# Kernel optimization log

Measured on AMD Instinct MI355X. Metric: run time of the kernel, lower is better.

Reference implementation:

```python
import jax, jax.numpy as jnp
import numpy as np
from jax import lax

NUM_HEADS = 8

def _conv2d(x, w, b, padding, rhs_dilation=(1, 1)):
    # x: NCHW, w: OIHW
    out = lax.conv_general_dilated(x, w, (1, 1), padding,
                                   rhs_dilation=rhs_dilation,
                                   dimension_numbers=('NCHW', 'OIHW', 'NCHW'))
    return out + b[None, :, None, None]

def _bn(x, scale, bias):
    # eval-mode batchnorm folded into per-channel affine
    return x * scale[None, :, None, None] + bias[None, :, None, None]

def setup_inputs() -> dict:
    key = jax.random.key(0)
    ks = jax.random.split(key, 12)
    B, C, H, W = 16, 256, 64, 64
    D = C // 2          # down_dim = 128
    Dq = D // 16        # weight bottleneck = 8
    return {
        'x':          jax.random.normal(ks[0], (B, C, H, W), jnp.float32),
        'conv2_w':    jax.random.normal(ks[1], (D, C, 3, 3), jnp.float32) * 0.02,
        'conv2_b':    jnp.zeros((D,), jnp.float32),
        'bn2_scale':  jax.random.uniform(ks[2], (D,), jnp.float32, 0.5, 1.5),
        'bn2_bias':   jax.random.normal(ks[3], (D,), jnp.float32) * 0.1,
        'temperature': jnp.ones((NUM_HEADS, 1, 1), jnp.float32),
        'w1_w':       jax.random.normal(ks[4], (Dq, D, 1, 1), jnp.float32) * 0.05,
        'w1_b':       jnp.zeros((Dq,), jnp.float32),
        'bnw_scale':  jax.random.uniform(ks[5], (Dq,), jnp.float32, 0.5, 1.5),
        'bnw_bias':   jax.random.normal(ks[6], (Dq,), jnp.float32) * 0.1,
        'w2_w':       jax.random.normal(ks[7], (D, Dq, 1, 1), jnp.float32) * 0.05,
        'w2_b':       jnp.zeros((D,), jnp.float32),
    }

def _l2_normalize_complex(z, eps=1e-12):
    # torch F.normalize on complex: divide by L2 norm of |z| along last dim
    n = jnp.sqrt(jnp.sum(jnp.real(z * jnp.conj(z)), axis=-1, keepdims=True))
    return z / jnp.maximum(n, eps)

def reference(x, conv2_w, conv2_b, bn2_scale, bn2_bias, temperature,
              w1_w, w1_b, bnw_scale, bnw_bias, w2_w, w2_b):
    # conv2 branch: 3x3 conv with dilation=3, padding=3 -> BN -> ReLU
    conv2 = jax.nn.relu(_bn(_conv2d(x, conv2_w, conv2_b,
                                    ((3, 3), (3, 3)), rhs_dilation=(3, 3)),
                            bn2_scale, bn2_bias))
    b, c, h, w = conv2.shape
    f = jnp.fft.fft2(conv2)                      # complex64, (b,c,h,w); q=k=v=tepqkv
    cp = c // NUM_HEADS
    qkv = f.reshape(b, NUM_HEADS, cp, h * w)     # 'b (head c) h w -> b head c (h w)'
    qn = _l2_normalize_complex(qkv)
    kn = qn
    # complex attention logits, temperature broadcast over heads
    attn = jnp.einsum('bhin,bhjn->bhij', qn, kn) * temperature.astype(attn_dtype := qn.dtype)
    # dual real/imag softmax reassembled into complex
    attn = lax.complex(jax.nn.softmax(attn.real, axis=-1),
                       jax.nn.softmax(attn.imag, axis=-1))
    out_f = jnp.einsum('bhij,bhjn->bhin', attn, qkv)
    # torch.fft.ifft2 default dims=(-2,-1): here over (c, h*w) axes — faithful
    out_f = jnp.abs(jnp.fft.ifft2(out_f)).reshape(b, c, h, w)
    # gating branch on real part of spectrum
    g = jax.nn.relu(_bn(_conv2d(f.real, w1_w, w1_b, ((0, 0), (0, 0))),
                        bnw_scale, bnw_bias))
    g = jax.nn.sigmoid(_conv2d(g, w2_w, w2_b, ((0, 0), (0, 0))))
    out_l = jnp.abs(jnp.fft.ifft2(g * f))        # ifft2 over (h, w)
    out = jnp.concatenate([out_f, out_l], axis=1)
    return out + x
```

## Files before the change

### kernel.cpp

```cpp
#include <hip/hip_runtime.h>

typedef unsigned short u16;
typedef short short8 __attribute__((ext_vector_type(8)));
typedef float f32x4 __attribute__((ext_vector_type(4)));

#define MF(a,b,c) __builtin_amdgcn_mfma_f32_16x16x32_bf16(a,b,c,0,0,0)

__device__ __forceinline__ float bu2f(u16 u){
  return __uint_as_float(((unsigned int)u) << 16);
}
__device__ __forceinline__ u16 f2bu(float f){
  unsigned int b = __float_as_uint(f);
  unsigned int r = (b + 0x7FFFu + ((b >> 16) & 1u)) >> 16;
  return (u16)r;
}
__device__ __forceinline__ void ld4a(float* d, const float* p){
  float4 v = *(const float4*)p;
  d[0]=v.x; d[1]=v.y; d[2]=v.z; d[3]=v.w;
}
__device__ __forceinline__ void st4(float* p, const float* s){
  *(float4*)p = make_float4(s[0], s[1], s[2], s[3]);
}
__device__ __forceinline__ void ld4b(float* d, const u16* p){
  ushort4 v = *(const ushort4*)p;
  d[0]=bu2f(v.x); d[1]=bu2f(v.y); d[2]=bu2f(v.z); d[3]=bu2f(v.w);
}
__device__ __forceinline__ void st4b(u16* p, const float* s){
  ushort4 v;
  v.x=f2bu(s[0]); v.y=f2bu(s[1]); v.z=f2bu(s[2]); v.w=f2bu(s[3]);
  *(ushort4*)p = v;
}
__device__ __forceinline__ ushort4 pk4(f32x4 v){
  ushort4 u; u.x=f2bu(v[0]); u.y=f2bu(v[1]); u.z=f2bu(v[2]); u.w=f2bu(v[3]); return u;
}
__device__ __forceinline__ short8 mulpk(short8 g, short8 f){
  short8 o;
  #pragma unroll
  for (int e = 0; e < 8; ++e)
    o[e] = (short)f2bu(bu2f((u16)g[e])*bu2f((u16)f[e]));
  return o;
}

#define TABF_RE   0
#define TABF_IM   4096
#define TABIF_RE  8192
#define TABIF_IM  12288
#define TABTW_RE  16384
#define TABTW_IM  20480
#define NORMS_OFF 24576
#define MMAT_OFF  26624
#define FLAG_OFF  92160
#define PRM_OFF   92224
#define WT_OFF    94848
#define DFT16_OFF 242304
#define F32_END   389760
#define P_CB   0
#define P_BNS  128
#define P_BNB  256
#define P_TEMP 384
#define P_W1   400
#define P_B1   1424
#define P_S1   1432
#define P_BB1  1440
#define P_W2   1456
#define P_B2   2480
#define BPLANE    8388608

__global__ void k_detect(const u16* __restrict__ xv, int* __restrict__ flag){
  const int t = threadIdx.x;
  int huge = 0;
  for (int i = 0; i < 16; ++i){
    u16 u = xv[(t*16 + i)*2];
    int e = (u >> 7) & 0xFF;
    huge += (e >= 0xC0) ? 1 : 0;
  }
  #pragma unroll
  for (int off = 32; off > 0; off >>= 1) huge += __shfl_down(huge, off, 64);
  if (t == 0) flag[0] = (huge >= 8) ? 1 : 0;
}

__global__ void k_tables(float* ws){
  int idx = blockIdx.x*256 + threadIdx.x;
  int j = idx >> 6, k = idx & 63;
  int jk = j*k;
  float s, c;
  sincospif(-(float)(jk & 63)/32.0f, &s, &c);
  ws[TABF_RE+idx] = c; ws[TABF_IM+idx] = s;
  sincospif((float)(jk & 63)/32.0f, &s, &c);
  ws[TABIF_RE+idx] = c*(1.f/64.f); ws[TABIF_IM+idx] = s*(1.f/64.f);
  sincospif((float)jk/2048.0f, &s, &c);
  ws[TABTW_RE+idx] = c; ws[TABTW_IM+idx] = s;
}

__global__ void k_dftprep(u16* __restrict__ m){
  int idx = blockIdx.x*256 + threadIdx.x;
  int j = idx >> 6, k = idx & 63;
  int jk = (j*k) & 63;
  float s, c;
  sincospif(-(float)jk/32.0f, &s, &c);
  m[idx]        = f2bu(c);
  m[4096+idx]   = f2bu(s);
  sincospif((float)jk/32.0f, &s, &c);
  m[8192+idx]   = f2bu(c*(1.f/64.f));
  m[12288+idx]  = f2bu(s*(1.f/64.f));
}

__global__ void k_pack(const void* cb, const void* bns, const void* bnb, const void* temp,
                       const void* w1, const void* b1, const void* s1, const void* bb1,
                       const void* w2, const void* b2,
                       const int* __restrict__ flg, float* __restrict__ P){
  const int t = threadIdx.x;
  const int f32 = *flg;
  if (f32){
    for (int i = t; i < 128; i += 256){
      P[P_CB+i]  = ((const float*)cb)[i];
      P[P_BNS+i] = ((const float*)bns)[i];
      P[P_BNB+i] = ((const float*)bnb)[i];
      P[P_B2+i]  = ((const float*)b2)[i];
    }
    for (int i = t; i < 1024; i += 256){
      P[P_W1+i] = ((const float*)w1)[i];
      P[P_W2+i] = ((const float*)w2)[i];
    }
    if (t < 8){
      P[P_TEMP+t] = ((const float*)temp)[t];
      P[P_B1+t]   = ((const float*)b1)[t];
      P[P_S1+t]   = ((const float*)s1)[t];
      P[P_BB1+t]  = ((const float*)bb1)[t];
    }
  } else {
    for (int i = t; i < 128; i += 256){
      P[P_CB+i]  = bu2f(((const u16*)cb)[i]);
      P[P_BNS+i] = bu2f(((const u16*)bns)[i]);
      P[P_BNB+i] = bu2f(((const u16*)bnb)[i]);
      P[P_B2+i]  = bu2f(((const u16*)b2)[i]);
    }
    for (int i = t; i < 1024; i += 256){
      P[P_W1+i] = bu2f(((const u16*)w1)[i]);
      P[P_W2+i] = bu2f(((const u16*)w2)[i]);
    }
    if (t < 8){
      P[P_TEMP+t] = bu2f(((const u16*)temp)[t]);
      P[P_B1+t]   = bu2f(((const u16*)b1)[t]);
      P[P_S1+t]   = bu2f(((const u16*)s1)[t]);
      P[P_BB1+t]  = bu2f(((const u16*)bb1)[t]);
    }
  }
}

__global__ void k_wprep2(const void* __restrict__ w, u16* __restrict__ wT2,
                         const float* __restrict__ prm, const int* __restrict__ flg){
  const int f32 = *flg;
  int U = blockIdx.x*256 + threadIdx.x;
  if (U < 294912){
    int j = U & 7;
    int E = U >> 3;
    int n = E & 127;
    int o = (E >> 7) & 3;
    int tc = E >> 9;
    int chunk = tc & 7, tap = tc >> 3;
    int c = chunk*32 + o*8 + j;
    int src = n*2304 + c*9 + tap;
    float v = f32 ? ((const float*)w)[src] : bu2f(((const u16*)w)[src]);
    wT2[U] = f2bu(v * prm[P_BNS + n]);
  }
}

__global__ __launch_bounds__(256) void k_trans(const void* __restrict__ x, u16* __restrict__ xt,
                                               const int* __restrict__ flg){
  __shared__ u16 L[256*66];
  const int t = threadIdx.x;
  const int b = blockIdx.x >> 6, h = blockIdx.x & 63;
  const int f32m = __builtin_amdgcn_readfirstlane(*flg);
  if (f32m){
    const float* xf = (const float*)x;
    for (int i = t; i < 16384; i += 256){
      int c = i >> 6, w = i & 63;
      L[c*66 + w] = f2bu(xf[((b*256 + c)*64 + h)*64 + w]);
    }
  } else {
    const u16* xb = (const u16*)x;
    for (int i = t; i < 16384; i += 256){
      int c = i >> 6, w = i & 63;
      L[c*66 + w] = xb[((b*256 + c)*64 + h)*64 + w];
    }
  }
  __syncthreads();
  u16* dst = xt + ((b*64 + h)*64)*256;
  for (int j = t; j < 16384; j += 256){
    int w = j >> 8, c = j & 255;
    dst[w*256 + c] = L[c*66 + w];
  }
}

__global__ __launch_bounds__(256) void k_cmm(const u16* __restrict__ xt, const u16* __restrict__ wT2,
                                             const float* __restrict__ prm, u16* __restrict__ A){
  __shared__ uint4 sm4[4096];
  const int t = threadIdx.x;
  const int bb = blockIdx.x >> 4;
  const int mtile = blockIdx.x & 15;
  const int h0 = mtile*4;
  const int lane = t & 63, wave = t >> 6;
  const int quad = lane >> 4, lr = lane & 15;

  f32x4 acc[4][8];
  #pragma unroll
  for (int mi = 0; mi < 4; ++mi)
    #pragma unroll
    for (int nt = 0; nt < 8; ++nt)
      acc[mi][nt] = (f32x4){0.f,0.f,0.f,0.f};

  const u16* smB = (const u16*)sm4;
  const short8 zz = {0,0,0,0,0,0,0,0};

  for (int tap = 0; tap < 9; ++tap){
    const int ky = tap/3, kx = tap - ky*3;
    __syncthreads();
    {
      const uint4* src = (const uint4*)(wT2 + tap*32768);
      #pragma unroll
      for (int i = 0; i < 16; ++i) sm4[t + 256*i] = src[t + 256*i];
    }
    __syncthreads();

    const int hg = h0 + wave + 3*ky - 3;
    const bool hok = ((unsigned)hg < 64u);
    const u16* abase = xt + ((bb*64 + hg)*64)*256 + quad*8;

    for (int chunk = 0; chunk < 8; ++chunk){
      short8 av[4];
      #pragma unroll
      for (int mi = 0; mi < 4; ++mi){
        const int wg = mi*16 + lr + 3*kx - 3;
        short8 v = zz;
        if (hok && ((unsigned)wg < 64u))
          v = *(const short8*)(abase + wg*256 + chunk*32);
        av[mi] = v;
      }
      short8 bv[8];
      #pragma unroll
      for (int nt = 0; nt < 8; ++nt)
        bv[nt] = *(const short8*)(smB + (chunk*512 + quad*128 + nt*16 + lr)*8);
      #pragma unroll
      for (int mi = 0; mi < 4; ++mi)
        #pragma unroll
        for (int nt = 0; nt < 8; ++nt)
          acc[mi][nt] = MF(av[mi], bv[nt], acc[mi][nt]);
    }
  }

  float* C = (float*)sm4;
  u16* outb = A + (bb*128)*4096 + mtile*256;
  __syncthreads();
  for (int nt = 0; nt < 8; ++nt){
    #pragma unroll
    for (int mi = 0; mi < 4; ++mi)
      #pragma unroll
      for (int r = 0; r < 4; ++r){
        int m = wave*64 + mi*16 + quad*4 + r;
        C[lr*261 + m] = acc[mi][nt][r];
      }
    __syncthreads();
    #pragma unroll
    for (int dd = 0; dd < 16; ++dd){
      int d = nt*16 + dd;
      float bi = prm[P_CB + d]*prm[P_BNS + d] + prm[P_BNB + d];
      float v = fmaxf(C[dd*261 + t] + bi, 0.f);
      outb[d*4096 + t] = f2bu(v);
    }
    __syncthreads();
  }
}

__global__ __launch_bounds__(256) void k_fft2_m(const u16* __restrict__ A, u16* __restrict__ Frb,
                                                u16* __restrict__ Fib, const u16* __restrict__ dft){
  __shared__ __align__(16) u16 TTr[64*72], TTi[64*72];
  const int bc = blockIdx.x, t = threadIdx.x;
  const int lane = t & 63, wave = t >> 6;
  const int quad = lane >> 4, lr = lane & 15;
  const u16* EFr = dft;
  const u16* EFi = dft + 4096;
  const u16* img = A + bc*4096;
  #pragma unroll
  for (int mi = 0; mi < 4; ++mi){
    f32x4 ar = {0.f,0.f,0.f,0.f}, ai = {0.f,0.f,0.f,0.f};
    #pragma unroll
    for (int ks = 0; ks < 2; ++ks){
      short8 av = *(const short8*)(img + (mi*16+lr)*64 + ks*32 + quad*8);
      short8 br = *(const short8*)(EFr + (wave*16+lr)*64 + ks*32 + quad*8);
      short8 bi = *(const short8*)(EFi + (wave*16+lr)*64 + ks*32 + quad*8);
      ar = MF(av, br, ar); ai = MF(av, bi, ai);
    }
    *(ushort4*)(TTr + (wave*16+lr)*72 + mi*16 + quad*4) = pk4(ar);
    *(ushort4*)(TTi + (wave*16+lr)*72 + mi*16 + quad*4) = pk4(ai);
  }
  __syncthreads();
  #pragma unroll
  for (int nt = 0; nt < 4; ++nt){
    f32x4 a1={0.f,0.f,0.f,0.f}, a2={0.f,0.f,0.f,0.f}, a3={0.f,0.f,0.f,0.f}, a4={0.f,0.f,0.f,0.f};
    #pragma unroll
    for (int ks = 0; ks < 2; ++ks){
      short8 tr = *(const short8*)(TTr + (wave*16+lr)*72 + ks*32 + quad*8);
      short8 ti = *(const short8*)(TTi + (wave*16+lr)*72 + ks*32 + quad*8);
      short8 br = *(const short8*)(EFr + (nt*16+lr)*64 + ks*32 + quad*8);
      short8 bi = *(const short8*)(EFi + (nt*16+lr)*64 + ks*32 + quad*8);
      a1 = MF(tr, br, a1); a2 = MF(ti, bi, a2);
      a3 = MF(tr, bi, a3); a4 = MF(ti, br, a4);
    }
    f32x4 fr, fi;
    #pragma unroll
    for (int r = 0; r < 4; ++r){ fr[r] = a1[r]-a2[r]; fi[r] = a3[r]+a4[r]; }
    const int flat = (nt*16+lr)*64 + wave*16 + quad*4;
    *(ushort4*)(Frb + bc*4096 + flat) = pk4(fr);
    *(ushort4*)(Fib + bc*4096 + flat) = pk4(fi);
  }
}

__global__ __launch_bounds__(256) void k_norms(const u16* __restrict__ Frb, const u16* __restrict__ Fib,
                                               float* __restrict__ norms){
  const int bc = blockIdx.x, t = threadIdx.x;
  const u16* pr = Frb + bc*4096;
  const u16* pi = Fib + bc*4096;
  float s = 0.f;
  for (int i = t*4; i < 4096; i += 1024){
    float a[4], b[4];
    ld4b(a, pr + i); ld4b(b, pi + i);
    #pragma unroll
    for (int k = 0; k < 4; ++k) s = fmaf(a[k],a[k],fmaf(b[k],b[k],s));
  }
  #pragma unroll
  for (int off = 32; off > 0; off >>= 1) s += __shfl_down(s, off, 64);
  __shared__ float red[4];
  if ((t & 63) == 0) red[t >> 6] = s;
  __syncthreads();
  if (t == 0){
    float tot = red[0]+red[1]+red[2]+red[3];
    norms[bc] = fmaxf(sqrtf(tot), 1e-12f);
  }
}

__global__ __launch_bounds__(256) void k_attn(const u16* __restrict__ Frb, const u16* __restrict__ Fib,
                                              const float* __restrict__ norms, const float* __restrict__ prm,
                                              float* __restrict__ wsM){
  __shared__ float SR[16][260];
  __shared__ float SI[16][260];
  __shared__ float AR[16][17], AI[16][17];
  const int bh = blockIdx.x;
  const int b = bh >> 3, h = bh & 7;
  const int t = threadIdx.x;
  const int tile = t & 15, part = t >> 4;
  const int i0 = (tile >> 2)*4, j0 = (tile & 3)*4;
  const u16* fr = Frb + (b*128 + h*16)*4096;
  const u16* fi = Fib + (b*128 + h*16)*4096;
  float gr[4][4] = {}, gi[4][4] = {};
  for (int nc = 0; nc < 16; ++nc){
    const int nb = nc*256;
    for (int idx = t; idx < 1024; idx += 256){
      int r = idx >> 6, col = (idx & 63)*4;
      float tmp[4];
      ld4b(tmp, fr + r*4096 + nb + col); st4(&SR[r][col], tmp);
      ld4b(tmp, fi + r*4096 + nb + col); st4(&SI[r][col], tmp);
    }
    __syncthreads();
    #pragma unroll
    for (int s = 0; s < 4; ++s){
      const int nn = part*16 + s*4;
      float arr[4][4], ari[4][4], brr[4][4], bri[4][4];
      #pragma unroll
      for (int i = 0; i < 4; ++i){
        ld4a(arr[i], &SR[i0+i][nn]);
        ld4a(ari[i], &SI[i0+i][nn]);
        ld4a(brr[i], &SR[j0+i][nn]);
        ld4a(bri[i], &SI[j0+i][nn]);
      }
      #pragma unroll
      for (int i = 0; i < 4; ++i)
        #pragma unroll
        for (int j = 0; j < 4; ++j)
          #pragma unroll
          for (int m = 0; m < 4; ++m){
            gr[i][j] += arr[i][m]*brr[j][m] - ari[i][m]*bri[j][m];
            gi[i][j] += arr[i][m]*bri[j][m] + ari[i][m]*brr[j][m];
          }
    }
    __syncthreads();
  }
  float* redR = &SR[0][0];
  float* redI = &SI[0][0];
  #pragma unroll
  for (int e = 0; e < 16; ++e){
    redR[t*16 + e] = gr[e>>2][e&3];
    redI[t*16 + e] = gi[e>>2][e&3];
  }
  __syncthreads();
  {
    const int tile2 = t >> 4, e2 = t & 15;
    float sr = 0.f, si = 0.f;
    for (int p = 0; p < 16; ++p){
      sr += redR[(p*16 + tile2)*16 + e2];
      si += redI[(p*16 + tile2)*16 + e2];
    }
    const int ii = (tile2 >> 2)*4 + (e2 >> 2);
    const int jj = (tile2 & 3)*4 + (e2 & 3);
    const float tm = prm[P_TEMP + h];
    const float sc = tm / (norms[b*128 + h*16 + ii] * norms[b*128 + h*16 + jj]);
    AR[ii][jj] = sr*sc;
    AI[ii][jj] = si*sc;
  }
  __syncthreads();
  if (t < 32){
    float* row = (t < 16) ? AR[t & 15] : AI[t & 15];
    float mx = row[0];
    for (int j2 = 1; j2 < 16; ++j2) mx = fmaxf(mx, row[j2]);
    float s = 0.f, e[16];
    for (int j2 = 0; j2 < 16; ++j2){ e[j2] = expf(row[j2] - mx); s += e[j2]; }
    float inv = 1.f/s;
    for (int j2 = 0; j2 < 16; ++j2) row[j2] = e[j2]*inv;
  }
  __syncthreads();
  {
    const int mi = t >> 4, mj = t & 15;
    float mr = 0.f, mim = 0.f;
    #pragma unroll
    for (int p = 0; p < 16; ++p){
      float sv, cv;
      sincospif((float)((mi*p) & 15)/8.0f, &sv, &cv);
      const float arv = AR[p][mj], aiv = AI[p][mj];
      mr  += cv*arv - sv*aiv;
      mim += cv*aiv + sv*arv;
    }
    wsM[bh*512 + t*2]     = mr*(1.f/16.f);
    wsM[bh*512 + t*2 + 1] = mim*(1.f/16.f);
  }
}

__global__ __launch_bounds__(256) void k_gate(const u16* __restrict__ Frb,
                                              const float* __restrict__ prm,
                                              u16* __restrict__ g){
  __shared__ float W1T[128][8];
  __shared__ float W2[128][8];
  __shared__ float B1v[8], S1v[8], BB1v[8];
  __shared__ float B2v[128];
  const int t = threadIdx.x;
  for (int i = t; i < 1024; i += 256){
    W1T[i & 127][i >> 7] = prm[P_W1 + i];
    W2[i >> 3][i & 7]    = prm[P_W2 + i];
  }
  if (t < 8){ B1v[t] = prm[P_B1+t]; S1v[t] = prm[P_S1+t]; BB1v[t] = prm[P_BB1+t]; }
  if (t < 128) B2v[t] = prm[P_B2+t];
  __syncthreads();
  const int pix = blockIdx.x*256 + t;
  const int b = pix >> 12, n = pix & 4095;
  const u16* fr = Frb + b*128*4096 + n;
  float q[8] = {};
  for (int c = 0; c < 128; ++c){
    const float v = bu2f(fr[c*4096]);
    float wa[4], wb[4];
    ld4a(wa, &W1T[c][0]); ld4a(wb, &W1T[c][4]);
    #pragma unroll
    for (int k = 0; k < 4; ++k){ q[k] = fmaf(wa[k], v, q[k]); q[4+k] = fmaf(wb[k], v, q[4+k]); }
  }
  float qa[8];
  #pragma unroll
  for (int k = 0; k < 8; ++k)
    qa[k] = fmaxf(fmaf(q[k] + B1v[k], S1v[k], BB1v[k]), 0.f);
  u16* grow = g + b*128*4096 + n;
  for (int c = 0; c < 128; ++c){
    float wa[4], wb[4];
    ld4a(wa, &W2[c][0]); ld4a(wb, &W2[c][4]);
    float acc = B2v[c];
    #pragma unroll
    for (int k = 0; k < 4; ++k) acc += wa[k]*qa[k] + wb[k]*qa[4+k];
    grow[c*4096] = f2bu(1.f/(1.f + expf(-acc)));
  }
}

__global__ __launch_bounds__(256) void k_outl_m(const u16* __restrict__ Frb, const u16* __restrict__ Fib,
                                                const u16* __restrict__ g, const void* __restrict__ x,
                                                float* __restrict__ out, const u16* __restrict__ dft,
                                                const int* __restrict__ flg){
  __shared__ __align__(16) u16 TTr[64*72], TTi[64*72];
  const int bc = blockIdx.x, t = threadIdx.x;
  const int b = bc >> 7, c = bc & 127;
  const int lane = t & 63, wave = t >> 6;
  const int quad = lane >> 4, lr = lane & 15;
  const int f32m = __builtin_amdgcn_readfirstlane(*flg);
  const u16* EIr = dft + 8192;
  const u16* EIi = dft + 12288;
  const u16* pg = g   + bc*4096;
  const u16* pr = Frb + bc*4096;
  const u16* pi = Fib + bc*4096;
  #pragma unroll
  for (int mi = 0; mi < 4; ++mi){
    f32x4 a1={0.f,0.f,0.f,0.f}, a2={0.f,0.f,0.f,0.f}, a3={0.f,0.f,0.f,0.f}, a4={0.f,0.f,0.f,0.f};
    #pragma unroll
    for (int ks = 0; ks < 2; ++ks){
      const int ao = (mi*16+lr)*64 + ks*32 + quad*8;
      short8 gv = *(const short8*)(pg + ao);
      short8 apr = mulpk(gv, *(const short8*)(pr + ao));
      short8 api = mulpk(gv, *(const short8*)(pi + ao));
      const int bo = (wave*16+lr)*64 + ks*32 + quad*8;
      short8 br = *(const short8*)(EIr + bo);
      short8 bi = *(const short8*)(EIi + bo);
      a1 = MF(apr, br, a1); a2 = MF(api, bi, a2);
      a3 = MF(apr, bi, a3); a4 = MF(api, br, a4);
    }
    f32x4 tr, ti;
    #pragma unroll
    for (int r = 0; r < 4; ++r){ tr[r] = a1[r]-a2[r]; ti[r] = a3[r]+a4[r]; }
    *(ushort4*)(TTr + (wave*16+lr)*72 + mi*16 + quad*4) = pk4(tr);
    *(ushort4*)(TTi + (wave*16+lr)*72 + mi*16 + quad*4) = pk4(ti);
  }
  __syncthreads();
  #pragma unroll
  for (int nt = 0; nt < 4; ++nt){
    f32x4 a1={0.f,0.f,0.f,0.f}, a2={0.f,0.f,0.f,0.f}, a3={0.f,0.f,0.f,0.f}, a4={0.f,0.f,0.f,0.f};
    #pragma unroll
    for (int ks = 0; ks < 2; ++ks){
      short8 tr = *(const short8*)(TTr + (wave*16+lr)*72 + ks*32 + quad*8);
      short8 ti = *(const short8*)(TTi + (wave*16+lr)*72 + ks*32 + quad*8);
      const int bo = (nt*16+lr)*64 + ks*32 + quad*8;
      short8 br = *(const short8*)(EIr + bo);
      short8 bi = *(const short8*)(EIi + bo);
      a1 = MF(tr, br, a1); a2 = MF(ti, bi, a2);
      a3 = MF(tr, bi, a3); a4 = MF(ti, br, a4);
    }
    const int o = (b*256 + 128 + c)*4096 + (nt*16+lr)*64 + wave*16 + quad*4;
    float xr[4];
    if (f32m) ld4a(xr, (const float*)x + o); else ld4b(xr, (const u16*)x + o);
    float ov[4];
    #pragma unroll
    for (int r = 0; r < 4; ++r){
      float yr = a1[r]-a2[r], yi = a3[r]+a4[r];
      ov[r] = sqrtf(yr*yr + yi*yi) + xr[r];
    }
    st4(out + o, ov);
  }
}

__global__ __launch_bounds__(256) void k_ifft4096_m(u16* __restrict__ Frb, u16* __restrict__ Fib,
                                                    const float* __restrict__ ws,
                                                    const u16* __restrict__ dft){
  __shared__ __align__(16) u16 A2Tr[64*72], A2Ti[64*72], Cr[64*72], Ci[64*72];
  const int bc = blockIdx.x, t = threadIdx.x;
  const int lane = t & 63, wave = t >> 6;
  const int quad = lane >> 4, lr = lane & 15;
  const u16* EIr = dft + 8192;
  const u16* EIi = dft + 12288;
  const float* twr = ws + TABTW_RE;
  const float* twi = ws + TABTW_IM;
  u16* fr = Frb + bc*4096;
  u16* fi = Fib + bc*4096;
  for (int i = t; i < 4096; i += 256){
    int n1 = i >> 6, n2 = i & 63;
    A2Tr[n2*72 + n1] = fr[i];
    A2Ti[n2*72 + n1] = fi[i];
  }
  __syncthreads();
  #pragma unroll
  for (int nt = 0; nt < 4; ++nt){
    f32x4 a1={0.f,0.f,0.f,0.f}, a2={0.f,0.f,0.f,0.f}, a3={0.f,0.f,0.f,0.f}, a4={0.f,0.f,0.f,0.f};
    #pragma unroll
    for (int ks = 0; ks < 2; ++ks){
      const int ao = (wave*16+lr)*64 + ks*32 + quad*8;
      short8 Ar = *(const short8*)(EIr + ao);
      short8 Ai = *(const short8*)(EIi + ao);
      short8 br = *(const short8*)(A2Tr + (nt*16+lr)*72 + ks*32 + quad*8);
      short8 bi = *(const short8*)(A2Ti + (nt*16+lr)*72 + ks*32 + quad*8);
      a1 = MF(Ar, br, a1); a2 = MF(Ai, bi, a2);
      a3 = MF(Ar, bi, a3); a4 = MF(Ai, br, a4);
    }
    #pragma unroll
    for (int r = 0; r < 4; ++r){
      const int k1 = wave*16 + quad*4 + r;
      const int n2 = nt*16 + lr;
      const float trv = a1[r]-a2[r], tiv = a3[r]+a4[r];
      const float wr = twr[k1*64 + n2], wi = twi[k1*64 + n2];
      Cr[k1*72 + n2] = f2bu(trv*wr - tiv*wi);
      Ci[k1*72 + n2] = f2bu(trv*wi + tiv*wr);
    }
  }
  __syncthreads();
  #pragma unroll
  for (int nt = 0; nt < 4; ++nt){
    f32x4 a1={0.f,0.f,0.f,0.f}, a2={0.f,0.f,0.f,0.f}, a3={0.f,0.f,0.f,0.f}, a4={0.f,0.f,0.f,0.f};
    #pragma unroll
    for (int ks = 0; ks < 2; ++ks){
      short8 Ar = *(const short8*)(Cr + (wave*16+lr)*72 + ks*32 + quad*8);
      short8 Ai = *(const short8*)(Ci + (wave*16+lr)*72 + ks*32 + quad*8);
      const int bo = (nt*16+lr)*64 + ks*32 + quad*8;
      short8 br = *(const short8*)(EIr + bo);
      short8 bi = *(const short8*)(EIi + bo);
      a1 = MF(Ar, br, a1); a2 = MF(Ai, bi, a2);
      a3 = MF(Ar, bi, a3); a4 = MF(Ai, br, a4);
    }
    f32x4 zr, zi;
    #pragma unroll
    for (int r = 0; r < 4; ++r){ zr[r] = a1[r]-a2[r]; zi[r] = a3[r]+a4[r]; }
    const int flat = (nt*16+lr)*64 + wave*16 + quad*4;
    *(ushort4*)(fr + flat) = pk4(zr);
    *(ushort4*)(fi + flat) = pk4(zi);
  }
}

__global__ __launch_bounds__(256) void k_outf(const u16* __restrict__ Zr, const u16* __restrict__ Zi,
                                              const float* __restrict__ wsM, const void* __restrict__ x,
                                              float* __restrict__ out, const int* __restrict__ flg){
  __shared__ float MreT[16][20], MimT[16][20];
  const int gb = blockIdx.x;
  const int bh = gb & 127, nch = gb >> 7;
  const int b = bh >> 3, h = bh & 7;
  const int t = threadIdx.x;
  const int f32m = __builtin_amdgcn_readfirstlane(*flg);
  {
    const int i = t >> 4, j = t & 15;
    MreT[j][i] = wsM[bh*512 + t*2];
    MimT[j][i] = wsM[bh*512 + t*2 + 1];
  }
  __syncthreads();
  const int i0 = (t & 3)*4;
  const int nn = nch*256 + (t >> 2)*4;
  const u16* zr = Zr + (b*128 + h*16)*4096 + nn;
  const u16* zi = Zi + (b*128 + h*16)*4096 + nn;
  float accr[4][4] = {}, acci[4][4] = {};
  #pragma unroll
  for (int j = 0; j < 16; ++j){
    float mr[4], mi[4], vr[4], vi[4];
    ld4a(mr, &MreT[j][i0]);
    ld4a(mi, &MimT[j][i0]);
    ld4b(vr, zr + j*4096);
    ld4b(vi, zi + j*4096);
    #pragma unroll
    for (int i = 0; i < 4; ++i)
      #pragma unroll
      for (int n = 0; n < 4; ++n){
        accr[i][n] += mr[i]*vr[n] - mi[i]*vi[n];
        acci[i][n] += mr[i]*vi[n] + mi[i]*vr[n];
      }
  }
  #pragma unroll
  for (int i = 0; i < 4; ++i){
    const int o = (b*256 + h*16 + i0 + i)*4096 + nn;
    float xr[4];
    if (f32m) ld4a(xr, (const float*)x + o); else ld4b(xr, (const u16*)x + o);
    float ov[4];
    #pragma unroll
    for (int n = 0; n < 4; ++n)
      ov[n] = sqrtf(accr[i][n]*accr[i][n] + acci[i][n]*acci[i][n]) + xr[n];
    st4(out + o, ov);
  }
}

extern "C" void kernel_launch(void* const* d_in, const int* in_sizes, int n_in,
                              void* d_out, int out_size, void* d_ws, size_t ws_size,
                              hipStream_t stream) {
  const void* x        = d_in[0];
  const void* conv2_w  = d_in[1];
  const void* conv2_b  = d_in[2];
  const void* bn2_s    = d_in[3];
  const void* bn2_b    = d_in[4];
  const void* temp     = d_in[5];
  const void* w1_w     = d_in[6];
  const void* w1_b     = d_in[7];
  const void* bnw_s    = d_in[8];
  const void* bnw_b    = d_in[9];
  const void* w2_w     = d_in[10];
  const void* w2_b     = d_in[11];
  float* out = (float*)d_out;
  float* wsf = (float*)d_ws;

  if (ws_size < (size_t)(F32_END*4) + 3u*(size_t)BPLANE*2u) return;

  int* flag = (int*)(wsf + FLAG_OFF);
  float* prm = wsf + PRM_OFF;
  u16* wT2 = (u16*)(wsf + WT_OFF);
  u16* dft = (u16*)(wsf + DFT16_OFF);
  u16* wsb = (u16*)(wsf + F32_END);
  u16* Frb = wsb;
  u16* Fib = wsb + BPLANE;
  u16* xt  = wsb;
  u16* Ab  = wsb + 2*BPLANE;
  u16* g   = Ab;

  k_detect<<<1, 64, 0, stream>>>((const u16*)x, flag);
  k_tables<<<16, 256, 0, stream>>>(wsf);
  k_dftprep<<<16, 256, 0, stream>>>(dft);
  k_pack<<<1, 256, 0, stream>>>(conv2_b, bn2_s, bn2_b, temp, w1_w, w1_b, bnw_s, bnw_b,
                                w2_w, w2_b, flag, prm);
  k_wprep2<<<1152, 256, 0, stream>>>(conv2_w, wT2, prm, flag);
  k_trans<<<1024, 256, 0, stream>>>(x, xt, flag);
  k_cmm<<<256, 256, 0, stream>>>(xt, wT2, prm, Ab);
  k_fft2_m<<<2048, 256, 0, stream>>>(Ab, Frb, Fib, dft);
  k_norms<<<2048, 256, 0, stream>>>(Frb, Fib, wsf + NORMS_OFF);
  k_attn<<<128, 256, 0, stream>>>(Frb, Fib, wsf + NORMS_OFF, prm, wsf + MMAT_OFF);
  k_gate<<<256, 256, 0, stream>>>(Frb, prm, g);
  k_outl_m<<<2048, 256, 0, stream>>>(Frb, Fib, g, x, out, dft, flag);
  k_ifft4096_m<<<2048, 256, 0, stream>>>(Frb, Fib, wsf, dft);
  k_outf<<<2048, 256, 0, stream>>>(Frb, Fib, wsf + MMAT_OFF, x, out, flag);
}
```

Baseline: 506.8 us.

## Compute attention Gram matrix with MFMA split-K, fold norms into diagonal

```diff
diff --git a/kernel.cpp b/kernel.cpp
--- a/kernel.cpp
+++ b/kernel.cpp
@@ -316,97 +316,63 @@
   }
 }
 
-__global__ __launch_bounds__(256) void k_norms(const u16* __restrict__ Frb, const u16* __restrict__ Fib,
-                                               float* __restrict__ norms){
-  const int bc = blockIdx.x, t = threadIdx.x;
-  const u16* pr = Frb + bc*4096;
-  const u16* pi = Fib + bc*4096;
-  float s = 0.f;
-  for (int i = t*4; i < 4096; i += 1024){
-    float a[4], b[4];
-    ld4b(a, pr + i); ld4b(b, pi + i);
-    #pragma unroll
-    for (int k = 0; k < 4; ++k) s = fmaf(a[k],a[k],fmaf(b[k],b[k],s));
-  }
-  #pragma unroll
-  for (int off = 32; off > 0; off >>= 1) s += __shfl_down(s, off, 64);
-  __shared__ float red[4];
-  if ((t & 63) == 0) red[t >> 6] = s;
-  __syncthreads();
-  if (t == 0){
-    float tot = red[0]+red[1]+red[2]+red[3];
-    norms[bc] = fmaxf(sqrtf(tot), 1e-12f);
-  }
-}
-
-__global__ __launch_bounds__(256) void k_attn(const u16* __restrict__ Frb, const u16* __restrict__ Fib,
-                                              const float* __restrict__ norms, const float* __restrict__ prm,
-                                              float* __restrict__ wsM){
-  __shared__ float SR[16][260];
-  __shared__ float SI[16][260];
-  __shared__ float AR[16][17], AI[16][17];
+__global__ __launch_bounds__(256) void k_attn1(const u16* __restrict__ Frb,
+                                               const u16* __restrict__ Fib,
+                                               float* __restrict__ part){
+  __shared__ float R[4][4][256];
+  const int blk = blockIdx.x;
+  const int bh = blk >> 4, chunk = blk & 15;
+  const int t = threadIdx.x, lane = t & 63, wave = t >> 6;
+  const int quad = lane >> 4, lr = lane & 15;
+  const u16* fr = Frb + bh*65536;
+  const u16* fi = Fib + bh*65536;
+  const int c0 = chunk*256 + wave*64;
+  f32x4 a1={0.f,0.f,0.f,0.f}, a2={0.f,0.f,0.f,0.f}, a3={0.f,0.f,0.f,0.f}, a4={0.f,0.f,0.f,0.f};
+  #pragma unroll
+  for (int ks = 0; ks < 2; ++ks){
+    const int off = lr*4096 + c0 + ks*32 + quad*8;
+    short8 ar = *(const short8*)(fr + off);
+    short8 ai = *(const short8*)(fi + off);
+    a1 = MF(ar, ar, a1); a2 = MF(ai, ai, a2);
+    a3 = MF(ar, ai, a3); a4 = MF(ai, ar, a4);
+  }
+  #pragma unroll
+  for (int r = 0; r < 4; ++r){
+    const int mn = (quad*4 + r)*16 + lr;
+    R[wave][0][mn] = a1[r];
+    R[wave][1][mn] = a2[r];
+    R[wave][2][mn] = a3[r];
+    R[wave][3][mn] = a4[r];
+  }
+  __syncthreads();
+  float* dst = part + blk*1024;
+  #pragma unroll
+  for (int q = 0; q < 4; ++q)
+    dst[q*256 + t] = R[0][q][t] + R[1][q][t] + R[2][q][t] + R[3][q][t];
+}
+
+__global__ __launch_bounds__(256) void k_attn2(const float* __restrict__ part,
+                                               const float* __restrict__ prm,
+                                               float* __restrict__ wsM){
+  __shared__ float AR[16][17], AI[16][17], NR[16];
   const int bh = blockIdx.x;
-  const int b = bh >> 3, h = bh & 7;
+  const int h = bh & 7;
   const int t = threadIdx.x;
-  const int tile = t & 15, part = t >> 4;
-  const int i0 = (tile >> 2)*4, j0 = (tile & 3)*4;
-  const u16* fr = Frb + (b*128 + h*16)*4096;
-  const u16* fi = Fib + (b*128 + h*16)*4096;
-  float gr[4][4] = {}, gi[4][4] = {};
-  for (int nc = 0; nc < 16; ++nc){
-    const int nb = nc*256;
-    for (int idx = t; idx < 1024; idx += 256){
-      int r = idx >> 6, col = (idx & 63)*4;
-      float tmp[4];
-      ld4b(tmp, fr + r*4096 + nb + col); st4(&SR[r][col], tmp);
-      ld4b(tmp, fi + r*4096 + nb + col); st4(&SI[r][col], tmp);
-    }
-    __syncthreads();
-    #pragma unroll
-    for (int s = 0; s < 4; ++s){
-      const int nn = part*16 + s*4;
-      float arr[4][4], ari[4][4], brr[4][4], bri[4][4];
-      #pragma unroll
-      for (int i = 0; i < 4; ++i){
-        ld4a(arr[i], &SR[i0+i][nn]);
-        ld4a(ari[i], &SI[i0+i][nn]);
-        ld4a(brr[i], &SR[j0+i][nn]);
-        ld4a(bri[i], &SI[j0+i][nn]);
-      }
-      #pragma unroll
-      for (int i = 0; i < 4; ++i)
-        #pragma unroll
-        for (int j = 0; j < 4; ++j)
-          #pragma unroll
-          for (int m = 0; m < 4; ++m){
-            gr[i][j] += arr[i][m]*brr[j][m] - ari[i][m]*bri[j][m];
-            gi[i][j] += arr[i][m]*bri[j][m] + ari[i][m]*brr[j][m];
-          }
-    }
-    __syncthreads();
-  }
-  float* redR = &SR[0][0];
-  float* redI = &SI[0][0];
-  #pragma unroll
-  for (int e = 0; e < 16; ++e){
-    redR[t*16 + e] = gr[e>>2][e&3];
-    redI[t*16 + e] = gi[e>>2][e&3];
-  }
-  __syncthreads();
-  {
-    const int tile2 = t >> 4, e2 = t & 15;
-    float sr = 0.f, si = 0.f;
-    for (int p = 0; p < 16; ++p){
-      sr += redR[(p*16 + tile2)*16 + e2];
-      si += redI[(p*16 + tile2)*16 + e2];
-    }
-    const int ii = (tile2 >> 2)*4 + (e2 >> 2);
-    const int jj = (tile2 & 3)*4 + (e2 & 3);
-    const float tm = prm[P_TEMP + h];
-    const float sc = tm / (norms[b*128 + h*16 + ii] * norms[b*128 + h*16 + jj]);
-    AR[ii][jj] = sr*sc;
-    AI[ii][jj] = si*sc;
-  }
+  const float* p = part + bh*16384;
+  float s1=0.f, s2=0.f, s3=0.f, s4=0.f;
+  #pragma unroll
+  for (int ch = 0; ch < 16; ++ch){
+    s1 += p[ch*1024 +       t];
+    s2 += p[ch*1024 + 256 + t];
+    s3 += p[ch*1024 + 512 + t];
+    s4 += p[ch*1024 + 768 + t];
+  }
+  const int m = t >> 4, n = t & 15;
+  if (m == n) NR[m] = fmaxf(sqrtf(fmaxf(s1 + s2, 0.f)), 1e-12f);
+  __syncthreads();
+  const float sc = prm[P_TEMP + h] / (NR[m]*NR[n]);
+  AR[m][n] = (s1 - s2)*sc;
+  AI[m][n] = (s3 + s4)*sc;
   __syncthreads();
   if (t < 32){
     float* row = (t < 16) ? AR[t & 15] : AI[t & 15];
@@ -422,10 +388,10 @@
     const int mi = t >> 4, mj = t & 15;
     float mr = 0.f, mim = 0.f;
     #pragma unroll
-    for (int p = 0; p < 16; ++p){
+    for (int pp = 0; pp < 16; ++pp){
       float sv, cv;
-      sincospif((float)((mi*p) & 15)/8.0f, &sv, &cv);
-      const float arv = AR[p][mj], aiv = AI[p][mj];
+      sincospif((float)((mi*pp) & 15)/8.0f, &sv, &cv);
+      const float arv = AR[pp][mj], aiv = AI[pp][mj];
       mr  += cv*arv - sv*aiv;
       mim += cv*aiv + sv*arv;
     }
@@ -681,6 +647,7 @@
   u16* xt  = wsb;
   u16* Ab  = wsb + 2*BPLANE;
   u16* g   = Ab;
+  float* part = (float*)Ab;
 
   k_detect<<<1, 64, 0, stream>>>((const u16*)x, flag);
   k_tables<<<16, 256, 0, stream>>>(wsf);
@@ -691,8 +658,8 @@
   k_trans<<<1024, 256, 0, stream>>>(x, xt, flag);
   k_cmm<<<256, 256, 0, stream>>>(xt, wT2, prm, Ab);
   k_fft2_m<<<2048, 256, 0, stream>>>(Ab, Frb, Fib, dft);
-  k_norms<<<2048, 256, 0, stream>>>(Frb, Fib, wsf + NORMS_OFF);
-  k_attn<<<128, 256, 0, stream>>>(Frb, Fib, wsf + NORMS_OFF, prm, wsf + MMAT_OFF);
+  k_attn1<<<2048, 256, 0, stream>>>(Frb, Fib, part);
+  k_attn2<<<128, 256, 0, stream>>>(part, prm, wsf + MMAT_OFF);
   k_gate<<<256, 256, 0, stream>>>(Frb, prm, g);
   k_outl_m<<<2048, 256, 0, stream>>>(Frb, Fib, g, x, out, dft, flag);
   k_ifft4096_m<<<2048, 256, 0, stream>>>(Frb, Fib, wsf, dft);
```

Result: faster. 438.3 us (-13.5%).
